# Kernel tuning notes

Hardware: AMD Instinct MI355X
Metric: run time of the kernel (lower is better)

The kernel has to match this reference:

```python
import jax, jax.numpy as jnp
import numpy as np

B, S, D, H = 8, 2048, 1024, 64

def setup_inputs() -> dict:
    key = jax.random.key(0)
    k1, k2, k3, k4 = jax.random.split(key, 4)
    idx = jax.random.normal(k1, (B, S, D), dtype=jnp.float32)
    # nn.Linear(D, H, bias=False) weights, stored as [D, H] for x @ W
    Wk = jax.random.normal(k2, (D, H), dtype=jnp.float32) * (1.0 / np.sqrt(D))
    Wq = jax.random.normal(k3, (D, H), dtype=jnp.float32) * (1.0 / np.sqrt(D))
    Wv = jax.random.normal(k4, (D, H), dtype=jnp.float32) * (1.0 / np.sqrt(D))
    return {"idx": idx, "Wk": Wk, "Wq": Wq, "Wv": Wv}

def reference(idx, Wk, Wq, Wv):
    b, s, d = idx.shape
    k = idx @ Wk  # [b, s, h]
    q = idx @ Wq
    v = idx @ Wv
    # NOTE: original scales by embedding_dim**-0.5, not head_size**-0.5
    wei = jnp.einsum('bqh,bkh->bqk', q, k) * (d ** -0.5)
    causal = jnp.tril(jnp.ones((s, s), dtype=bool))
    wei = jnp.where(causal, wei, -jnp.inf)
    attn = jax.nn.softmax(wei, axis=-1)  # dropout p=0.0 -> identity
    return jnp.einsum('bqk,bkh->bqh', attn, v)
```

## Files before the change

### kernel.cpp

```cpp
#include <hip/hip_runtime.h>

typedef __attribute__((ext_vector_type(8))) short short8;
typedef __attribute__((ext_vector_type(4))) short short4v;
typedef __attribute__((ext_vector_type(4))) float f32x4;

#define MFMA_16x16x32_BF16(A, B, C) __builtin_amdgcn_mfma_f32_16x16x32_bf16(A, B, C, 0, 0, 0)

__device__ __forceinline__ unsigned short f2bf(float x) {
    unsigned int u = __builtin_bit_cast(unsigned int, x);
    u = (u + 0x7FFFu + ((u >> 16) & 1u)) >> 16;
    return (unsigned short)u;
}

__global__ __launch_bounds__(256) void wconv_kernel(const float* __restrict__ Wk,
                                                    const float* __restrict__ Wq,
                                                    const float* __restrict__ Wv,
                                                    unsigned short* __restrict__ Wt) {
    const int n = blockIdx.x;
    const float* W = (n < 64) ? Wk : (n < 128) ? Wq : Wv;
    const int col = n & 63;
    const int sw = (n & 7) << 3;
    for (int k = threadIdx.x; k < 1024; k += 256) {
        const int kd = (k & ~56) | ((k ^ sw) & 56);
        Wt[(size_t)n * 1024 + kd] = f2bf(W[(size_t)k * 64 + col]);
    }
}

__global__ __launch_bounds__(512, 4) void proj_kernel(const float* __restrict__ X,
                                                      const unsigned short* __restrict__ Wt,
                                                      unsigned short* __restrict__ Kb,
                                                      unsigned short* __restrict__ Qb,
                                                      unsigned short* __restrict__ Vtg) {
    __shared__ __attribute__((aligned(16))) unsigned short Wl[2][192 * 64];
    __shared__ __attribute__((aligned(16))) unsigned short Al[2][32 * 72];
    const int t = threadIdx.x;
    const int w = t >> 6, lane = t & 63, lr = lane & 15, g = lane >> 4;
    const int rw = w >> 2, cw = w & 3;
    const int r0 = blockIdx.x * 32;

    f32x4 acc[3] = {};

    const int ar = t >> 4, ac = (t & 15) * 4;
    const float* xsrc = X + (size_t)(r0 + ar) * 1024 + ac;

    float4 fly = *(const float4*)xsrc;
    uint2 aw;
    aw.x = (unsigned)f2bf(fly.x) | ((unsigned)f2bf(fly.y) << 16);
    aw.y = (unsigned)f2bf(fly.z) | ((unsigned)f2bf(fly.w) << 16);
    *(uint2*)&Al[0][ar * 72 + ac] = aw;
#pragma unroll
    for (int i = 0; i < 3; ++i) {
        const int q = t + 512 * i;
        const unsigned short* src = Wt + (size_t)(q >> 3) * 1024 + (q & 7) * 8;
        __builtin_amdgcn_global_load_lds((const __attribute__((address_space(1))) void*)src,
                                         (__attribute__((address_space(3))) void*)&Wl[0][q * 8],
                                         16, 0, 0);
    }
    __builtin_amdgcn_sched_barrier(0);
    fly = *(const float4*)(xsrc + 64);
    asm volatile("s_waitcnt vmcnt(1) lgkmcnt(0)" ::: "memory");
    __builtin_amdgcn_s_barrier();

    for (int t16 = 0; t16 < 16; ++t16) {
        const int cur = t16 & 1;
        if (t16 < 15) {
            aw.x = (unsigned)f2bf(fly.x) | ((unsigned)f2bf(fly.y) << 16);
            aw.y = (unsigned)f2bf(fly.z) | ((unsigned)f2bf(fly.w) << 16);
            *(uint2*)&Al[cur ^ 1][ar * 72 + ac] = aw;
            const int k1 = (t16 + 1) * 64;
#pragma unroll
            for (int i = 0; i < 3; ++i) {
                const int q = t + 512 * i;
                const unsigned short* src = Wt + (size_t)(q >> 3) * 1024 + k1 + (q & 7) * 8;
                __builtin_amdgcn_global_load_lds((const __attribute__((address_space(1))) void*)src,
                                                 (__attribute__((address_space(3))) void*)&Wl[cur ^ 1][q * 8],
                                                 16, 0, 0);
            }
            __builtin_amdgcn_sched_barrier(0);
            const int anext = (t16 + 2 < 15) ? (t16 + 2) : 15;
            fly = *(const float4*)(xsrc + anext * 64);
        }

        short8 af[2];
        af[0] = *(const short8*)&Al[cur][(16 * rw + lr) * 72 + 8 * g];
        af[1] = *(const short8*)&Al[cur][(16 * rw + lr) * 72 + 32 + 8 * g];
#pragma unroll
        for (int c = 0; c < 3; ++c) {
            const int row = 48 * cw + 16 * c + lr;
#pragma unroll
            for (int sub = 0; sub < 2; ++sub) {
                const int cs = (4 * sub + g) ^ (lr & 7);
                short8 wf = *(const short8*)&Wl[cur][row * 64 + cs * 8];
                acc[c] = MFMA_16x16x32_BF16(af[sub], wf, acc[c]);
            }
        }
        asm volatile("s_waitcnt vmcnt(1) lgkmcnt(0)" ::: "memory");
        __builtin_amdgcn_s_barrier();
    }

    const int bb = r0 >> 11;
    const int sb0 = (r0 & 2047) + 16 * rw + 4 * g;
    const int row = r0 + 16 * rw + 4 * g;
#pragma unroll
    for (int i = 0; i < 3; ++i) {
        const int cg = cw * 3 + i;
        if (cg < 4) {
#pragma unroll
            for (int r = 0; r < 4; ++r)
                Kb[(size_t)(row + r) * 64 + 16 * cg + lr] = f2bf(acc[i][r]);
        } else if (cg < 8) {
#pragma unroll
            for (int r = 0; r < 4; ++r)
                Qb[(size_t)(row + r) * 64 + 16 * (cg - 4) + lr] = f2bf(acc[i][r]);
        } else {
            const int h = 16 * (cg - 8) + lr;
            uint2 e;
            e.x = (unsigned)f2bf(acc[i][0]) | ((unsigned)f2bf(acc[i][1]) << 16);
            e.y = (unsigned)f2bf(acc[i][2]) | ((unsigned)f2bf(acc[i][3]) << 16);
            *(uint2*)(Vtg + (size_t)bb * 64 * 2048 + (size_t)h * 2048 + sb0) = e;
        }
    }
}

__global__ __launch_bounds__(1024, 4) void attn_kernel(const unsigned short* __restrict__ Kb,
                                                       const unsigned short* __restrict__ Qb,
                                                       const unsigned short* __restrict__ Vtg,
                                                       float* __restrict__ out) {
    __shared__ __attribute__((aligned(16))) float Pacc[16][32][68];
    __shared__ float Pml[2][16][32];

    const int t = threadIdx.x;
    const int w = t >> 6, lane = t & 63;
    const int lr = lane & 15, g = lane >> 4;
    const int p = blockIdx.x, b = blockIdx.y;
    const int band = w >> 3, wi = w & 7;
    const int nb = band ? (p + 1) : (64 - p);
    const int q0 = band ? p * 32 : (63 - p) * 32;
    const size_t rowbase = (size_t)b * 2048;
    const size_t vbase = (size_t)b * 64 * 2048;
    const float NEG_INF = -__builtin_inff();
    const float SCALE2 = 0.03125f * 1.4426950408889634f;

    short8 qf[2][2];
#pragma unroll
    for (int sub = 0; sub < 2; ++sub)
#pragma unroll
        for (int hh = 0; hh < 2; ++hh)
            qf[sub][hh] = *(const short8*)(Qb + (rowbase + q0 + 16 * sub + lr) * 64 + 32 * hh + 8 * g);

    f32x4 acc[2][4] = {};
    float m2[2] = {NEG_INF, NEG_INF};
    float ls[2] = {0.f, 0.f};

    const int s0 = (wi * nb) >> 3, s1 = ((wi + 1) * nb) >> 3;

    for (int s = s0; s < s1; ++s) {
        const int kv0 = s * 32;
        short8 kf[2][2];
#pragma unroll
        for (int f = 0; f < 2; ++f)
#pragma unroll
            for (int hh = 0; hh < 2; ++hh)
                kf[f][hh] = *(const short8*)(Kb + (rowbase + kv0 + 16 * f + lr) * 64 + 32 * hh + 8 * g);
        short8 vf[4];
#pragma unroll
        for (int fh = 0; fh < 4; ++fh) {
            const unsigned short* vp = Vtg + vbase + (size_t)(16 * fh + lr) * 2048 + kv0 + 4 * g;
            short4v v0 = *(const short4v*)vp;
            short4v v1 = *(const short4v*)(vp + 16);
            short8 vv;
            vv[0] = v0[0]; vv[1] = v0[1]; vv[2] = v0[2]; vv[3] = v0[3];
            vv[4] = v1[0]; vv[5] = v1[1]; vv[6] = v1[2]; vv[7] = v1[3];
            vf[fh] = vv;
        }
#pragma unroll
        for (int sub = 0; sub < 2; ++sub) {
            f32x4 sv[2];
#pragma unroll
            for (int f = 0; f < 2; ++f) {
                f32x4 x = {};
                x = MFMA_16x16x32_BF16(kf[f][0], qf[sub][0], x);
                x = MFMA_16x16x32_BF16(kf[f][1], qf[sub][1], x);
                sv[f] = x;
            }
            const int q = q0 + 16 * sub + lr;
            float pvv[8], tmax = NEG_INF;
#pragma unroll
            for (int f = 0; f < 2; ++f)
#pragma unroll
                for (int r = 0; r < 4; ++r) {
                    int kp = kv0 + 16 * f + 4 * g + r;
                    float sc = sv[f][r] * SCALE2;
                    sc = (kp <= q) ? sc : NEG_INF;
                    pvv[4 * f + r] = sc;
                    tmax = fmaxf(tmax, sc);
                }
            tmax = fmaxf(tmax, __shfl_xor(tmax, 16));
            tmax = fmaxf(tmax, __shfl_xor(tmax, 32));
            float mnew = fmaxf(m2[sub], tmax);
            float alpha = exp2f(m2[sub] - mnew);
            float psum = 0.f;
            short8 pf;
#pragma unroll
            for (int e = 0; e < 8; ++e) {
                float pe = exp2f(pvv[e] - mnew);
                psum += pe;
                pf[e] = (short)f2bf(pe);
            }
            psum += __shfl_xor(psum, 16);
            psum += __shfl_xor(psum, 32);
            ls[sub] = ls[sub] * alpha + psum;
            m2[sub] = mnew;
#pragma unroll
            for (int fh = 0; fh < 4; ++fh) {
                acc[sub][fh][0] *= alpha; acc[sub][fh][1] *= alpha;
                acc[sub][fh][2] *= alpha; acc[sub][fh][3] *= alpha;
                acc[sub][fh] = MFMA_16x16x32_BF16(vf[fh], pf, acc[sub][fh]);
            }
        }
    }

    {
        const int slot = band * 8 + wi;
#pragma unroll
        for (int sub = 0; sub < 2; ++sub) {
#pragma unroll
            for (int fh = 0; fh < 4; ++fh)
                *(f32x4*)&Pacc[slot][16 * sub + lr][16 * fh + 4 * g] = acc[sub][fh];
            if (g == 0) {
                Pml[0][slot][16 * sub + lr] = m2[sub];
                Pml[1][slot][16 * sub + lr] = ls[sub];
            }
        }
    }
    __syncthreads();

    {
        const int tb = t >> 9, t2 = t & 511;
        const int qq = t2 & 31, hb = (t2 >> 5) * 4;
        float mw[8], M = NEG_INF;
#pragma unroll
        for (int wv = 0; wv < 8; ++wv) {
            mw[wv] = Pml[0][tb * 8 + wv][qq];
            M = fmaxf(M, mw[wv]);
        }
        float wgt[8], L = 0.f;
#pragma unroll
        for (int wv = 0; wv < 8; ++wv) {
            wgt[wv] = exp2f(mw[wv] - M);
            L += wgt[wv] * Pml[1][tb * 8 + wv][qq];
        }
        f32x4 o = {};
#pragma unroll
        for (int wv = 0; wv < 8; ++wv)
            o += wgt[wv] * *(const f32x4*)&Pacc[tb * 8 + wv][qq][hb];
        o *= (1.f / L);
        const int qb = tb ? p * 32 : (63 - p) * 32;
        *(f32x4*)(out + (rowbase + qb + qq) * 64 + hb) = o;
    }
}

extern "C" void kernel_launch(void* const* d_in, const int* in_sizes, int n_in,
                              void* d_out, int out_size, void* d_ws, size_t ws_size,
                              hipStream_t stream) {
    const float* X  = (const float*)d_in[0];
    const float* Wk = (const float*)d_in[1];
    const float* Wq = (const float*)d_in[2];
    const float* Wv = (const float*)d_in[3];

    unsigned short* Wt  = (unsigned short*)d_ws;
    unsigned short* Kb  = Wt + 192 * 1024;
    unsigned short* Qb  = Kb + 16384 * 64;
    unsigned short* Vtg = Qb + 16384 * 64;
    float* out = (float*)d_out;

    wconv_kernel<<<dim3(192), dim3(256), 0, stream>>>(Wk, Wq, Wv, Wt);
    proj_kernel<<<dim3(512), dim3(512), 0, stream>>>(X, Wt, Kb, Qb, Vtg);
    attn_kernel<<<dim3(32, 8), dim3(1024), 0, stream>>>(Kb, Qb, Vtg, out);
}
```

Baseline: 54.97 us.

## Double projection row tile and halve attention block with prefetched KV

The projection kernel now handles 64 rows per block instead of 32, so each staged weight tile feeds two MFMA row groups, and it launches half as many blocks. The attention kernel drops from 1024 to 512 threads: each wave walks a contiguous share of the combined high and low causal bands and prefetches the next K/V tile into registers. This aims to cut weight reloads and balance causal work across waves. The cost is higher register pressure, lower occupancy, and fewer waves per block to hide latency.

```diff
diff --git a/kernel.cpp b/kernel.cpp
--- a/kernel.cpp
+++ b/kernel.cpp
@@ -26,28 +26,33 @@
     }
 }
 
-__global__ __launch_bounds__(512, 4) void proj_kernel(const float* __restrict__ X,
+__global__ __launch_bounds__(512, 2) void proj_kernel(const float* __restrict__ X,
                                                       const unsigned short* __restrict__ Wt,
                                                       unsigned short* __restrict__ Kb,
                                                       unsigned short* __restrict__ Qb,
                                                       unsigned short* __restrict__ Vtg) {
     __shared__ __attribute__((aligned(16))) unsigned short Wl[2][192 * 64];
-    __shared__ __attribute__((aligned(16))) unsigned short Al[2][32 * 72];
+    __shared__ __attribute__((aligned(16))) unsigned short Al[2][64 * 72];
     const int t = threadIdx.x;
     const int w = t >> 6, lane = t & 63, lr = lane & 15, g = lane >> 4;
     const int rw = w >> 2, cw = w & 3;
-    const int r0 = blockIdx.x * 32;
-
-    f32x4 acc[3] = {};
-
-    const int ar = t >> 4, ac = (t & 15) * 4;
-    const float* xsrc = X + (size_t)(r0 + ar) * 1024 + ac;
-
-    float4 fly = *(const float4*)xsrc;
-    uint2 aw;
-    aw.x = (unsigned)f2bf(fly.x) | ((unsigned)f2bf(fly.y) << 16);
-    aw.y = (unsigned)f2bf(fly.z) | ((unsigned)f2bf(fly.w) << 16);
-    *(uint2*)&Al[0][ar * 72 + ac] = aw;
+    const int r0 = blockIdx.x * 64;
+
+    f32x4 acc[2][3] = {};
+
+    const int ar = t >> 3, aj = t & 7;
+    const float* xsrc = X + (size_t)(r0 + ar) * 1024 + aj * 8;
+
+    {
+        float4 a0 = *(const float4*)xsrc;
+        float4 a1 = *(const float4*)(xsrc + 4);
+        uint4 aw;
+        aw.x = (unsigned)f2bf(a0.x) | ((unsigned)f2bf(a0.y) << 16);
+        aw.y = (unsigned)f2bf(a0.z) | ((unsigned)f2bf(a0.w) << 16);
+        aw.z = (unsigned)f2bf(a1.x) | ((unsigned)f2bf(a1.y) << 16);
+        aw.w = (unsigned)f2bf(a1.z) | ((unsigned)f2bf(a1.w) << 16);
+        *(uint4*)&Al[0][ar * 72 + aj * 8] = aw;
+    }
 #pragma unroll
     for (int i = 0; i < 3; ++i) {
         const int q = t + 512 * i;
@@ -57,16 +62,20 @@
                                          16, 0, 0);
     }
     __builtin_amdgcn_sched_barrier(0);
-    fly = *(const float4*)(xsrc + 64);
-    asm volatile("s_waitcnt vmcnt(1) lgkmcnt(0)" ::: "memory");
+    float4 fly0 = *(const float4*)(xsrc + 64);
+    float4 fly1 = *(const float4*)(xsrc + 68);
+    asm volatile("s_waitcnt vmcnt(2) lgkmcnt(0)" ::: "memory");
     __builtin_amdgcn_s_barrier();
 
     for (int t16 = 0; t16 < 16; ++t16) {
         const int cur = t16 & 1;
         if (t16 < 15) {
-            aw.x = (unsigned)f2bf(fly.x) | ((unsigned)f2bf(fly.y) << 16);
-            aw.y = (unsigned)f2bf(fly.z) | ((unsigned)f2bf(fly.w) << 16);
-            *(uint2*)&Al[cur ^ 1][ar * 72 + ac] = aw;
+            uint4 aw;
+            aw.x = (unsigned)f2bf(fly0.x) | ((unsigned)f2bf(fly0.y) << 16);
+            aw.y = (unsigned)f2bf(fly0.z) | ((unsigned)f2bf(fly0.w) << 16);
+            aw.z = (unsigned)f2bf(fly1.x) | ((unsigned)f2bf(fly1.y) << 16);
+            aw.w = (unsigned)f2bf(fly1.z) | ((unsigned)f2bf(fly1.w) << 16);
+            *(uint4*)&Al[cur ^ 1][ar * 72 + aj * 8] = aw;
             const int k1 = (t16 + 1) * 64;
 #pragma unroll
             for (int i = 0; i < 3; ++i) {
@@ -78,12 +87,16 @@
             }
             __builtin_amdgcn_sched_barrier(0);
             const int anext = (t16 + 2 < 15) ? (t16 + 2) : 15;
-            fly = *(const float4*)(xsrc + anext * 64);
-        }
-
-        short8 af[2];
-        af[0] = *(const short8*)&Al[cur][(16 * rw + lr) * 72 + 8 * g];
-        af[1] = *(const short8*)&Al[cur][(16 * rw + lr) * 72 + 32 + 8 * g];
+            fly0 = *(const float4*)(xsrc + anext * 64);
+            fly1 = *(const float4*)(xsrc + anext * 64 + 4);
+        }
+
+        short8 af[2][2];
+#pragma unroll
+        for (int t_ = 0; t_ < 2; ++t_)
+#pragma unroll
+            for (int sub = 0; sub < 2; ++sub)
+                af[t_][sub] = *(const short8*)&Al[cur][(32 * rw + 16 * t_ + lr) * 72 + 32 * sub + 8 * g];
 #pragma unroll
         for (int c = 0; c < 3; ++c) {
             const int row = 48 * cw + 16 * c + lr;
@@ -91,41 +104,47 @@
             for (int sub = 0; sub < 2; ++sub) {
                 const int cs = (4 * sub + g) ^ (lr & 7);
                 short8 wf = *(const short8*)&Wl[cur][row * 64 + cs * 8];
-                acc[c] = MFMA_16x16x32_BF16(af[sub], wf, acc[c]);
-            }
-        }
-        asm volatile("s_waitcnt vmcnt(1) lgkmcnt(0)" ::: "memory");
-        __builtin_amdgcn_s_barrier();
+                acc[0][c] = MFMA_16x16x32_BF16(af[0][sub], wf, acc[0][c]);
+                acc[1][c] = MFMA_16x16x32_BF16(af[1][sub], wf, acc[1][c]);
+            }
+        }
+        if (t16 < 15) {
+            asm volatile("s_waitcnt vmcnt(2) lgkmcnt(0)" ::: "memory");
+            __builtin_amdgcn_s_barrier();
+        }
     }
 
     const int bb = r0 >> 11;
-    const int sb0 = (r0 & 2047) + 16 * rw + 4 * g;
-    const int row = r0 + 16 * rw + 4 * g;
-#pragma unroll
-    for (int i = 0; i < 3; ++i) {
-        const int cg = cw * 3 + i;
-        if (cg < 4) {
-#pragma unroll
-            for (int r = 0; r < 4; ++r)
-                Kb[(size_t)(row + r) * 64 + 16 * cg + lr] = f2bf(acc[i][r]);
-        } else if (cg < 8) {
-#pragma unroll
-            for (int r = 0; r < 4; ++r)
-                Qb[(size_t)(row + r) * 64 + 16 * (cg - 4) + lr] = f2bf(acc[i][r]);
-        } else {
-            const int h = 16 * (cg - 8) + lr;
-            uint2 e;
-            e.x = (unsigned)f2bf(acc[i][0]) | ((unsigned)f2bf(acc[i][1]) << 16);
-            e.y = (unsigned)f2bf(acc[i][2]) | ((unsigned)f2bf(acc[i][3]) << 16);
-            *(uint2*)(Vtg + (size_t)bb * 64 * 2048 + (size_t)h * 2048 + sb0) = e;
-        }
-    }
-}
-
-__global__ __launch_bounds__(1024, 4) void attn_kernel(const unsigned short* __restrict__ Kb,
-                                                       const unsigned short* __restrict__ Qb,
-                                                       const unsigned short* __restrict__ Vtg,
-                                                       float* __restrict__ out) {
+#pragma unroll
+    for (int t_ = 0; t_ < 2; ++t_) {
+        const int row = r0 + 32 * rw + 16 * t_ + 4 * g;
+        const int sb0 = (r0 & 2047) + 32 * rw + 16 * t_ + 4 * g;
+#pragma unroll
+        for (int i = 0; i < 3; ++i) {
+            const int cg = cw * 3 + i;
+            if (cg < 4) {
+#pragma unroll
+                for (int r = 0; r < 4; ++r)
+                    Kb[(size_t)(row + r) * 64 + 16 * cg + lr] = f2bf(acc[t_][i][r]);
+            } else if (cg < 8) {
+#pragma unroll
+                for (int r = 0; r < 4; ++r)
+                    Qb[(size_t)(row + r) * 64 + 16 * (cg - 4) + lr] = f2bf(acc[t_][i][r]);
+            } else {
+                const int h = 16 * (cg - 8) + lr;
+                uint2 e;
+                e.x = (unsigned)f2bf(acc[t_][i][0]) | ((unsigned)f2bf(acc[t_][i][1]) << 16);
+                e.y = (unsigned)f2bf(acc[t_][i][2]) | ((unsigned)f2bf(acc[t_][i][3]) << 16);
+                *(uint2*)(Vtg + (size_t)bb * 64 * 2048 + (size_t)h * 2048 + sb0) = e;
+            }
+        }
+    }
+}
+
+__global__ __launch_bounds__(512, 2) void attn_kernel(const unsigned short* __restrict__ Kb,
+                                                      const unsigned short* __restrict__ Qb,
+                                                      const unsigned short* __restrict__ Vtg,
+                                                      float* __restrict__ out) {
     __shared__ __attribute__((aligned(16))) float Pacc[16][32][68];
     __shared__ float Pml[2][16][32];
 
@@ -133,36 +152,21 @@
     const int w = t >> 6, lane = t & 63;
     const int lr = lane & 15, g = lane >> 4;
     const int p = blockIdx.x, b = blockIdx.y;
-    const int band = w >> 3, wi = w & 7;
-    const int nb = band ? (p + 1) : (64 - p);
-    const int q0 = band ? p * 32 : (63 - p) * 32;
+    const int nhi = 64 - p;
+    const int q0h = (63 - p) * 32, q0l = p * 32;
     const size_t rowbase = (size_t)b * 2048;
     const size_t vbase = (size_t)b * 64 * 2048;
     const float NEG_INF = -__builtin_inff();
     const float SCALE2 = 0.03125f * 1.4426950408889634f;
 
-    short8 qf[2][2];
-#pragma unroll
-    for (int sub = 0; sub < 2; ++sub)
-#pragma unroll
-        for (int hh = 0; hh < 2; ++hh)
-            qf[sub][hh] = *(const short8*)(Qb + (rowbase + q0 + 16 * sub + lr) * 64 + 32 * hh + 8 * g);
-
-    f32x4 acc[2][4] = {};
-    float m2[2] = {NEG_INF, NEG_INF};
-    float ls[2] = {0.f, 0.f};
-
-    const int s0 = (wi * nb) >> 3, s1 = ((wi + 1) * nb) >> 3;
-
-    for (int s = s0; s < s1; ++s) {
-        const int kv0 = s * 32;
-        short8 kf[2][2];
+    const int s0 = (w * 65) >> 3, s1 = ((w + 1) * 65) >> 3;
+
+    auto loadKV = [&](int kv0, short8 (&kf)[2][2], short8 (&vf)[4]) {
 #pragma unroll
         for (int f = 0; f < 2; ++f)
 #pragma unroll
             for (int hh = 0; hh < 2; ++hh)
                 kf[f][hh] = *(const short8*)(Kb + (rowbase + kv0 + 16 * f + lr) * 64 + 32 * hh + 8 * g);
-        short8 vf[4];
 #pragma unroll
         for (int fh = 0; fh < 4; ++fh) {
             const unsigned short* vp = Vtg + vbase + (size_t)(16 * fh + lr) * 2048 + kv0 + 4 * g;
@@ -173,6 +177,11 @@
             vv[4] = v1[0]; vv[5] = v1[1]; vv[6] = v1[2]; vv[7] = v1[3];
             vf[fh] = vv;
         }
+    };
+
+    auto stepc = [&](int kv0, int q0, const short8 (&qf)[2][2],
+                     const short8 (&kf)[2][2], const short8 (&vf)[4],
+                     f32x4 (&acc)[2][4], float (&m2)[2], float (&ls)[2]) {
 #pragma unroll
         for (int sub = 0; sub < 2; ++sub) {
             f32x4 sv[2];
@@ -218,26 +227,80 @@
                 acc[sub][fh] = MFMA_16x16x32_BF16(vf[fh], pf, acc[sub][fh]);
             }
         }
-    }
+    };
+
+    auto runband = [&](int sBeg, int sEnd, int base, int q0, const short8 (&qf)[2][2],
+                       f32x4 (&acc)[2][4], float (&m2)[2], float (&ls)[2]) {
+        int s = sBeg;
+        if (s >= sEnd) return;
+        short8 kfA[2][2], vfA[4], kfB[2][2], vfB[4];
+        loadKV((s - base) * 32, kfA, vfA);
+        __builtin_amdgcn_sched_barrier(0);
+        while (true) {
+            if (s + 1 < sEnd) {
+                loadKV((s + 1 - base) * 32, kfB, vfB);
+                __builtin_amdgcn_sched_barrier(0);
+            }
+            stepc((s - base) * 32, q0, qf, kfA, vfA, acc, m2, ls);
+            ++s; if (s >= sEnd) break;
+            if (s + 1 < sEnd) {
+                loadKV((s + 1 - base) * 32, kfA, vfA);
+                __builtin_amdgcn_sched_barrier(0);
+            }
+            stepc((s - base) * 32, q0, qf, kfB, vfB, acc, m2, ls);
+            ++s; if (s >= sEnd) break;
+        }
+    };
 
     {
-        const int slot = band * 8 + wi;
+        short8 qfH[2][2];
+#pragma unroll
+        for (int sub = 0; sub < 2; ++sub)
+#pragma unroll
+            for (int hh = 0; hh < 2; ++hh)
+                qfH[sub][hh] = *(const short8*)(Qb + (rowbase + q0h + 16 * sub + lr) * 64 + 32 * hh + 8 * g);
+        f32x4 accH[2][4] = {};
+        float mH[2] = {NEG_INF, NEG_INF}, lH[2] = {0.f, 0.f};
+        const int e = (s1 < nhi) ? s1 : nhi;
+        runband(s0, e, 0, q0h, qfH, accH, mH, lH);
 #pragma unroll
         for (int sub = 0; sub < 2; ++sub) {
 #pragma unroll
             for (int fh = 0; fh < 4; ++fh)
-                *(f32x4*)&Pacc[slot][16 * sub + lr][16 * fh + 4 * g] = acc[sub][fh];
+                *(f32x4*)&Pacc[w][16 * sub + lr][16 * fh + 4 * g] = accH[sub][fh];
             if (g == 0) {
-                Pml[0][slot][16 * sub + lr] = m2[sub];
-                Pml[1][slot][16 * sub + lr] = ls[sub];
+                Pml[0][w][16 * sub + lr] = mH[sub];
+                Pml[1][w][16 * sub + lr] = lH[sub];
+            }
+        }
+    }
+    {
+        short8 qfL[2][2];
+#pragma unroll
+        for (int sub = 0; sub < 2; ++sub)
+#pragma unroll
+            for (int hh = 0; hh < 2; ++hh)
+                qfL[sub][hh] = *(const short8*)(Qb + (rowbase + q0l + 16 * sub + lr) * 64 + 32 * hh + 8 * g);
+        f32x4 accL[2][4] = {};
+        float mL[2] = {NEG_INF, NEG_INF}, lL[2] = {0.f, 0.f};
+        const int sBeg = (s0 > nhi) ? s0 : nhi;
+        runband(sBeg, s1, nhi, q0l, qfL, accL, mL, lL);
+#pragma unroll
+        for (int sub = 0; sub < 2; ++sub) {
+#pragma unroll
+            for (int fh = 0; fh < 4; ++fh)
+                *(f32x4*)&Pacc[8 + w][16 * sub + lr][16 * fh + 4 * g] = accL[sub][fh];
+            if (g == 0) {
+                Pml[0][8 + w][16 * sub + lr] = mL[sub];
+                Pml[1][8 + w][16 * sub + lr] = lL[sub];
             }
         }
     }
     __syncthreads();
 
     {
-        const int tb = t >> 9, t2 = t & 511;
-        const int qq = t2 & 31, hb = (t2 >> 5) * 4;
+        const int tb = t >> 8, t2 = t & 255;
+        const int qq = t2 & 31, hb = (t2 >> 5) * 8;
         float mw[8], M = NEG_INF;
 #pragma unroll
         for (int wv = 0; wv < 8; ++wv) {
@@ -250,13 +313,20 @@
             wgt[wv] = exp2f(mw[wv] - M);
             L += wgt[wv] * Pml[1][tb * 8 + wv][qq];
         }
-        f32x4 o = {};
-#pragma unroll
-        for (int wv = 0; wv < 8; ++wv)
-            o += wgt[wv] * *(const f32x4*)&Pacc[tb * 8 + wv][qq][hb];
-        o *= (1.f / L);
-        const int qb = tb ? p * 32 : (63 - p) * 32;
-        *(f32x4*)(out + (rowbase + qb + qq) * 64 + hb) = o;
+        f32x4 o0 = {}, o1 = {};
+#pragma unroll
+        for (int wv = 0; wv < 8; ++wv) {
+            f32x4 a0 = *(const f32x4*)&Pacc[tb * 8 + wv][qq][hb];
+            f32x4 a1 = *(const f32x4*)&Pacc[tb * 8 + wv][qq][hb + 4];
+            o0 += wgt[wv] * a0;
+            o1 += wgt[wv] * a1;
+        }
+        const float invL = 1.f / L;
+        o0 *= invL; o1 *= invL;
+        const int q0 = tb ? q0l : q0h;
+        float* op = out + (rowbase + q0 + qq) * 64 + hb;
+        *(f32x4*)op = o0;
+        *(f32x4*)(op + 4) = o1;
     }
 }
 
@@ -275,6 +345,6 @@
     float* out = (float*)d_out;
 
     wconv_kernel<<<dim3(192), dim3(256), 0, stream>>>(Wk, Wq, Wv, Wt);
-    proj_kernel<<<dim3(512), dim3(512), 0, stream>>>(X, Wt, Kb, Qb, Vtg);
-    attn_kernel<<<dim3(32, 8), dim3(1024), 0, stream>>>(Kb, Qb, Vtg, out);
-}
+    proj_kernel<<<dim3(256), dim3(512), 0, stream>>>(X, Wt, Kb, Qb, Vtg);
+    attn_kernel<<<dim3(32, 8), dim3(512), 0, stream>>>(Kb, Qb, Vtg, out);
+}
```

Result: slower. 59.78 us (+8.8%).
